# Performance work log

Measured on AMD Instinct MI355X. Metric: run time of the kernel, lower is better.

## Reference

```python
import jax, jax.numpy as jnp
import numpy as np

TOPK = 2


def setup_inputs() -> dict:
    key = jax.random.key(0)
    k1, k2 = jax.random.split(key)
    B, N, D, E, C = 4, 2048, 2048, 8, 512
    token_inputs = jax.random.normal(k1, (B, N, D), dtype=jnp.float32)
    # bottleneck_in.weight.t() stacked over experts: [E, D, C]; scaled like a real init
    bottleneck_weights = jax.random.normal(k2, (E, D, C), dtype=jnp.float32) * 0.02
    return {
        "token_inputs": token_inputs,
        "bottleneck_weights": bottleneck_weights,
        "expert_capacity": 640,
    }


def _routing(router_probs, expert_capacity, topk):
    # router_probs: [B, N, E]
    B, N, E = router_probs.shape
    _, expert_indices = jax.lax.top_k(router_probs, topk)      # [B, N, topk]
    idx = jnp.transpose(expert_indices, (0, 2, 1)).reshape(B, topk * N)
    expert_mask = jax.nn.one_hot(idx, E, dtype=jnp.int32)       # [B, topk*N, E]
    token_priority = jnp.cumsum(expert_mask, axis=1) * expert_mask - 1
    token_priority = token_priority.reshape(B, topk, N, E)
    token_priority = jnp.transpose(token_priority, (0, 2, 1, 3))  # [B, N, topk, E]
    token_priority = jnp.max(token_priority, axis=2)              # [B, N, E]
    # one-hot over capacity; negative (-1) and >= capacity priorities map to all-zero rows
    cap_range = jnp.arange(expert_capacity, dtype=jnp.int32)
    dispatch = (token_priority[..., None] == cap_range).astype(jnp.float32)  # [B,N,E,C]
    combine = router_probs[..., None] * dispatch                            # [B,N,E,C]
    return dispatch, combine


def reference(token_inputs, bottleneck_weights, expert_capacity):
    # activation_cache: [B, N, E, Cb]
    activation_cache = jnp.einsum("bnd,edc->bnec", token_inputs, bottleneck_weights)
    router_logits = jnp.sqrt(jnp.sum(activation_cache * activation_cache, axis=-1))  # [B,N,E]
    router_probs = jax.nn.softmax(router_logits, axis=-1)
    dispatch, combine = _routing(router_probs, expert_capacity, TOPK)
    return jnp.stack([dispatch, combine], axis=0)  # [2, B, N, E, capacity]
```

## Files before the change

kernel.cpp:

```cpp
#include <hip/hip_runtime.h>
#include <math.h>

constexpr int Bb = 4, Nn = 2048, Dd = 2048, Ee = 8, Cbn = 512;
constexpr int Mm = Bb * Nn;
constexpr int Ncols = Ee * Cbn;

typedef _Float16 half8 __attribute__((ext_vector_type(8)));
typedef _Float16 half4v __attribute__((ext_vector_type(4)));
typedef float floatx16 __attribute__((ext_vector_type(16)));

#define GLL16(g, l)                                                     \
  __builtin_amdgcn_global_load_lds(                                     \
      (const __attribute__((address_space(1))) void*)(g),               \
      (__attribute__((address_space(3))) void*)(l), 16, 0, 0)

__global__ __launch_bounds__(256) void split_x(const float* __restrict__ X,
                                               _Float16* __restrict__ hi,
                                               _Float16* __restrict__ lo) {
  int i = (blockIdx.x * 256 + threadIdx.x) * 4;
  float4 v = *(const float4*)(X + i);
  half4v h, l;
  h.x = (_Float16)v.x; l.x = (_Float16)(v.x - (float)h.x);
  h.y = (_Float16)v.y; l.y = (_Float16)(v.y - (float)h.y);
  h.z = (_Float16)v.z; l.z = (_Float16)(v.z - (float)h.z);
  h.w = (_Float16)v.w; l.w = (_Float16)(v.w - (float)h.w);
  *(half4v*)(hi + i) = h;
  *(half4v*)(lo + i) = l;
}

__global__ __launch_bounds__(256) void transpose_w(const float* __restrict__ W,
                                                   _Float16* __restrict__ WThi,
                                                   _Float16* __restrict__ WTlo) {
  const int kt = blockIdx.x;
  const int ct = blockIdx.y;
  const int e = blockIdx.z;
  __shared__ _Float16 thi[64][68];
  __shared__ _Float16 tlo[64][68];
  const int tx = threadIdx.x & 15, ty = threadIdx.x >> 4;
  const float* src = W + ((size_t)(e * 2048 + kt * 64)) * 512 + ct * 64;
#pragma unroll
  for (int p = 0; p < 4; ++p) {
    int kk = ty + p * 16;
    float4 v = *(const float4*)(src + (size_t)kk * 512 + tx * 4);
    _Float16 h;
    h = (_Float16)v.x; thi[tx * 4 + 0][kk] = h; tlo[tx * 4 + 0][kk] = (_Float16)(v.x - (float)h);
    h = (_Float16)v.y; thi[tx * 4 + 1][kk] = h; tlo[tx * 4 + 1][kk] = (_Float16)(v.y - (float)h);
    h = (_Float16)v.z; thi[tx * 4 + 2][kk] = h; tlo[tx * 4 + 2][kk] = (_Float16)(v.z - (float)h);
    h = (_Float16)v.w; thi[tx * 4 + 3][kk] = h; tlo[tx * 4 + 3][kk] = (_Float16)(v.w - (float)h);
  }
  __syncthreads();
  _Float16* dh = WThi + ((size_t)(e * 512 + ct * 64)) * 2048 + kt * 64;
  _Float16* dl = WTlo + ((size_t)(e * 512 + ct * 64)) * 2048 + kt * 64;
#pragma unroll
  for (int p = 0; p < 4; ++p) {
    int cc = ty + p * 16;
    half4v h, l;
    h.x = thi[cc][tx * 4 + 0]; l.x = tlo[cc][tx * 4 + 0];
    h.y = thi[cc][tx * 4 + 1]; l.y = tlo[cc][tx * 4 + 1];
    h.z = thi[cc][tx * 4 + 2]; l.z = tlo[cc][tx * 4 + 2];
    h.w = thi[cc][tx * 4 + 3]; l.w = tlo[cc][tx * 4 + 3];
    *(half4v*)(dh + (size_t)cc * 2048 + tx * 4) = h;
    *(half4v*)(dl + (size_t)cc * 2048 + tx * 4) = l;
  }
}

__global__ __launch_bounds__(256) void gemm_mfma(const _Float16* __restrict__ Xhi,
                                                 const _Float16* __restrict__ Xlo,
                                                 const _Float16* __restrict__ WThi,
                                                 const _Float16* __restrict__ WTlo,
                                                 float* __restrict__ partial) {
  const int mtile = blockIdx.x;
  const int ntile = blockIdx.y;
  const int tid = threadIdx.x;
  const int wave = tid >> 6, lane = tid & 63;
  const int wm = wave >> 1, wn = wave & 1;
  const int h = lane >> 5;

  __shared__ __align__(16) char lds[32768];
  char* ldsAhi = lds;
  char* ldsAlo = lds + 8192;
  char* ldsBhi = lds + 16384;
  char* ldsBlo = lds + 24576;

  const int lr = lane >> 2;
  const int cpos = lane & 3;
  const int cg = cpos ^ ((lr >> 1) & 3);
  const int r0 = wave * 32 + lr;
  const int r1 = r0 + 16;
  const _Float16* xh0 = Xhi + (size_t)(mtile * 128 + r0) * 2048 + cg * 8;
  const _Float16* xh1 = Xhi + (size_t)(mtile * 128 + r1) * 2048 + cg * 8;
  const _Float16* xl0 = Xlo + (size_t)(mtile * 128 + r0) * 2048 + cg * 8;
  const _Float16* xl1 = Xlo + (size_t)(mtile * 128 + r1) * 2048 + cg * 8;
  const _Float16* wh0 = WThi + (size_t)(ntile * 128 + r0) * 2048 + cg * 8;
  const _Float16* wh1 = WThi + (size_t)(ntile * 128 + r1) * 2048 + cg * 8;
  const _Float16* wl0 = WTlo + (size_t)(ntile * 128 + r0) * 2048 + cg * 8;
  const _Float16* wl1 = WTlo + (size_t)(ntile * 128 + r1) * 2048 + cg * 8;
  const int lq0 = wave * 2048;
  const int lq1 = lq0 + 1024;

  const int rA0 = wm * 64 + (lane & 31);
  const int rA1 = rA0 + 32;
  const int rB0 = wn * 64 + (lane & 31);
  const int rB1 = rB0 + 32;
  auto foff = [&](int r, int s) {
    return r * 64 + (((s * 2 + h) ^ ((r >> 1) & 3)) << 4);
  };
  const int oA0[2] = {foff(rA0, 0), foff(rA0, 1)};
  const int oA1[2] = {foff(rA1, 0), foff(rA1, 1)};
  const int oB0[2] = {foff(rB0, 0), foff(rB0, 1)};
  const int oB1[2] = {foff(rB1, 0), foff(rB1, 1)};

  floatx16 acc00 = {}, acc01 = {}, acc10 = {}, acc11 = {};

  for (int kt = 0; kt < 64; ++kt) {
    const int k0 = kt * 32;
    GLL16(xh0 + k0, ldsAhi + lq0);
    GLL16(xh1 + k0, ldsAhi + lq1);
    GLL16(xl0 + k0, ldsAlo + lq0);
    GLL16(xl1 + k0, ldsAlo + lq1);
    GLL16(wh0 + k0, ldsBhi + lq0);
    GLL16(wh1 + k0, ldsBhi + lq1);
    GLL16(wl0 + k0, ldsBlo + lq0);
    GLL16(wl1 + k0, ldsBlo + lq1);
    __syncthreads();
#pragma unroll
    for (int s = 0; s < 2; ++s) {
      half8 ah0 = *(const half8*)(ldsAhi + oA0[s]);
      half8 ah1 = *(const half8*)(ldsAhi + oA1[s]);
      half8 al0 = *(const half8*)(ldsAlo + oA0[s]);
      half8 al1 = *(const half8*)(ldsAlo + oA1[s]);
      half8 bh0 = *(const half8*)(ldsBhi + oB0[s]);
      half8 bh1 = *(const half8*)(ldsBhi + oB1[s]);
      half8 bl0 = *(const half8*)(ldsBlo + oB0[s]);
      half8 bl1 = *(const half8*)(ldsBlo + oB1[s]);
      acc00 = __builtin_amdgcn_mfma_f32_32x32x16_f16(ah0, bh0, acc00, 0, 0, 0);
      acc00 = __builtin_amdgcn_mfma_f32_32x32x16_f16(ah0, bl0, acc00, 0, 0, 0);
      acc00 = __builtin_amdgcn_mfma_f32_32x32x16_f16(al0, bh0, acc00, 0, 0, 0);
      acc01 = __builtin_amdgcn_mfma_f32_32x32x16_f16(ah0, bh1, acc01, 0, 0, 0);
      acc01 = __builtin_amdgcn_mfma_f32_32x32x16_f16(ah0, bl1, acc01, 0, 0, 0);
      acc01 = __builtin_amdgcn_mfma_f32_32x32x16_f16(al0, bh1, acc01, 0, 0, 0);
      acc10 = __builtin_amdgcn_mfma_f32_32x32x16_f16(ah1, bh0, acc10, 0, 0, 0);
      acc10 = __builtin_amdgcn_mfma_f32_32x32x16_f16(ah1, bl0, acc10, 0, 0, 0);
      acc10 = __builtin_amdgcn_mfma_f32_32x32x16_f16(al1, bh0, acc10, 0, 0, 0);
      acc11 = __builtin_amdgcn_mfma_f32_32x32x16_f16(ah1, bh1, acc11, 0, 0, 0);
      acc11 = __builtin_amdgcn_mfma_f32_32x32x16_f16(ah1, bl1, acc11, 0, 0, 0);
      acc11 = __builtin_amdgcn_mfma_f32_32x32x16_f16(al1, bh1, acc11, 0, 0, 0);
    }
    __syncthreads();
  }

  float myv = 0.f;
#pragma unroll
  for (int i = 0; i < 2; ++i) {
    const floatx16& c0 = i ? acc10 : acc00;
    const floatx16& c1 = i ? acc11 : acc01;
#pragma unroll
    for (int reg = 0; reg < 16; ++reg) {
      float v = c0[reg] * c0[reg] + c1[reg] * c1[reg];
#pragma unroll
      for (int m = 1; m <= 16; m <<= 1) v += __shfl_xor(v, m, 64);
      if ((lane & 31) == i * 16 + reg) myv = v;
    }
  }
  {
    const int i = (lane & 31) >> 4;
    const int reg = lane & 15;
    const int row = i * 32 + (reg & 3) + 8 * (reg >> 2) + 4 * h;
    const int token = mtile * 128 + wm * 64 + row;
    const int slice = ntile * 2 + wn;
    partial[(size_t)slice * Mm + token] = myv;
  }
}

__global__ void route_kernel(const float* __restrict__ partial,
                             int* __restrict__ idx1, int* __restrict__ idx2,
                             float* __restrict__ p1, float* __restrict__ p2) {
  int t = blockIdx.x * blockDim.x + threadIdx.x;
  if (t >= Mm) return;
  float l[Ee];
  float mx = -1e30f;
#pragma unroll
  for (int e = 0; e < Ee; ++e) {
    float s = 0.f;
#pragma unroll
    for (int u = 0; u < 8; ++u) s += partial[(size_t)(e * 8 + u) * Mm + t];
    l[e] = sqrtf(s);
    mx = fmaxf(mx, l[e]);
  }
  float p[Ee];
  float s = 0.f;
#pragma unroll
  for (int e = 0; e < Ee; ++e) {
    p[e] = expf(l[e] - mx);
    s += p[e];
  }
  float inv = 1.f / s;
  int i1 = 0;
  float b1 = l[0];
#pragma unroll
  for (int e = 1; e < Ee; ++e)
    if (l[e] > b1) { b1 = l[e]; i1 = e; }
  int i2 = -1;
  float b2 = -1e30f;
#pragma unroll
  for (int e = 0; e < Ee; ++e)
    if (e != i1 && l[e] > b2) { b2 = l[e]; i2 = e; }
  idx1[t] = i1;
  idx2[t] = i2;
  p1[t] = p[i1] * inv;
  p2[t] = p[i2] * inv;
}

__global__ void scan_kernel(const int* __restrict__ idx1,
                            const int* __restrict__ idx2,
                            int* __restrict__ prios) {
  const int b = blockIdx.x;
  const int tid = threadIdx.x;
  __shared__ int cnts[256][8];
  int cnt[8] = {0, 0, 0, 0, 0, 0, 0, 0};
  int eloc[16];
  const int base_p = tid * 16;
#pragma unroll
  for (int i = 0; i < 16; ++i) {
    int p = base_p + i;
    int k = p >> 11;
    int n = p & (Nn - 1);
    int e = (k == 0 ? idx1 : idx2)[b * Nn + n];
    eloc[i] = e;
    cnt[e]++;
  }
#pragma unroll
  for (int e = 0; e < 8; ++e) cnts[tid][e] = cnt[e];
  __syncthreads();
  if (tid < 8) {
    int run = 0;
    for (int i = 0; i < 256; ++i) {
      int v = cnts[i][tid];
      cnts[i][tid] = run;
      run += v;
    }
  }
  __syncthreads();
  int base[8];
#pragma unroll
  for (int e = 0; e < 8; ++e) base[e] = cnts[tid][e];
#pragma unroll
  for (int i = 0; i < 16; ++i) {
    int e = eloc[i];
    prios[b * 2 * Nn + base_p + i] = base[e]++;
  }
}

__global__ void zero_kernel(float4* __restrict__ out, int n4) {
  int i = blockIdx.x * blockDim.x + threadIdx.x;
  if (i < n4) out[i] = make_float4(0.f, 0.f, 0.f, 0.f);
}

__global__ void scatter_kernel(const int* __restrict__ idx1,
                               const int* __restrict__ idx2,
                               const float* __restrict__ p1,
                               const float* __restrict__ p2,
                               const int* __restrict__ prios,
                               float* __restrict__ out, int cap) {
  int t = blockIdx.x * blockDim.x + threadIdx.x;
  if (t >= Mm) return;
  int b = t >> 11;
  int n = t & (Nn - 1);
  size_t disp = (size_t)t * Ee * cap;
  size_t comb = disp + (size_t)Mm * Ee * cap;
  {
    int e = idx1[t];
    int p = prios[b * 2 * Nn + n];
    if (p < cap) {
      out[disp + (size_t)e * cap + p] = 1.f;
      out[comb + (size_t)e * cap + p] = p1[t];
    }
  }
  {
    int e = idx2[t];
    int p = prios[b * 2 * Nn + Nn + n];
    if (p < cap) {
      out[disp + (size_t)e * cap + p] = 1.f;
      out[comb + (size_t)e * cap + p] = p2[t];
    }
  }
}

extern "C" void kernel_launch(void* const* d_in, const int* in_sizes, int n_in,
                              void* d_out, int out_size, void* d_ws, size_t ws_size,
                              hipStream_t stream) {
  const float* X = (const float*)d_in[0];
  const float* W = (const float*)d_in[1];
  float* out = (float*)d_out;
  const int cap = out_size / (2 * Bb * Nn * Ee);

  char* ws = (char*)d_ws;
  _Float16* Xhi = (_Float16*)ws;
  _Float16* Xlo = (_Float16*)(ws + 33554432ull);
  _Float16* WThi = (_Float16*)(ws + 67108864ull);
  _Float16* WTlo = (_Float16*)(ws + 83886080ull);
  float* partial = (float*)(ws + 100663296ull);
  int* idx1 = (int*)(ws + 102760448ull);
  int* idx2 = idx1 + Mm;
  float* p1 = (float*)(idx2 + Mm);
  float* p2 = p1 + Mm;
  int* prios = (int*)(p2 + Mm);

  split_x<<<(Mm * Dd) / 1024, 256, 0, stream>>>(X, Xhi, Xlo);
  transpose_w<<<dim3(32, 8, 8), 256, 0, stream>>>(W, WThi, WTlo);
  gemm_mfma<<<dim3(64, 32), 256, 0, stream>>>(Xhi, Xlo, WThi, WTlo, partial);
  route_kernel<<<Mm / 256, 256, 0, stream>>>(partial, idx1, idx2, p1, p2);
  scan_kernel<<<Bb, 256, 0, stream>>>(idx1, idx2, prios);
  const int n4 = out_size / 4;
  zero_kernel<<<(n4 + 255) / 256, 256, 0, stream>>>((float4*)out, n4);
  scatter_kernel<<<Mm / 256, 256, 0, stream>>>(idx1, idx2, p1, p2, prios, out, cap);
}
```

Before: 820.1 us.

## Double-buffer GEMM LDS, fuse routing into scan, fuse zero-fill with scatter

```diff
diff --git a/kernel.cpp b/kernel.cpp
--- a/kernel.cpp
+++ b/kernel.cpp
@@ -3,7 +3,6 @@
 
 constexpr int Bb = 4, Nn = 2048, Dd = 2048, Ee = 8, Cbn = 512;
 constexpr int Mm = Bb * Nn;
-constexpr int Ncols = Ee * Cbn;
 
 typedef _Float16 half8 __attribute__((ext_vector_type(8)));
 typedef _Float16 half4v __attribute__((ext_vector_type(4)));
@@ -76,11 +75,7 @@
   const int wm = wave >> 1, wn = wave & 1;
   const int h = lane >> 5;
 
-  __shared__ __align__(16) char lds[32768];
-  char* ldsAhi = lds;
-  char* ldsAlo = lds + 8192;
-  char* ldsBhi = lds + 16384;
-  char* ldsBlo = lds + 24576;
+  __shared__ __align__(16) char lds[2][32768];
 
   const int lr = lane >> 2;
   const int cpos = lane & 3;
@@ -112,27 +107,38 @@
 
   floatx16 acc00 = {}, acc01 = {}, acc10 = {}, acc11 = {};
 
+  auto issue = [&](int kt, int buf) {
+    const int k0 = kt * 32;
+    char* L = lds[buf];
+    GLL16(xh0 + k0, L + lq0);
+    GLL16(xh1 + k0, L + lq1);
+    GLL16(xl0 + k0, L + 8192 + lq0);
+    GLL16(xl1 + k0, L + 8192 + lq1);
+    GLL16(wh0 + k0, L + 16384 + lq0);
+    GLL16(wh1 + k0, L + 16384 + lq1);
+    GLL16(wl0 + k0, L + 24576 + lq0);
+    GLL16(wl1 + k0, L + 24576 + lq1);
+  };
+
+  issue(0, 0);
+  int p = 0;
   for (int kt = 0; kt < 64; ++kt) {
-    const int k0 = kt * 32;
-    GLL16(xh0 + k0, ldsAhi + lq0);
-    GLL16(xh1 + k0, ldsAhi + lq1);
-    GLL16(xl0 + k0, ldsAlo + lq0);
-    GLL16(xl1 + k0, ldsAlo + lq1);
-    GLL16(wh0 + k0, ldsBhi + lq0);
-    GLL16(wh1 + k0, ldsBhi + lq1);
-    GLL16(wl0 + k0, ldsBlo + lq0);
-    GLL16(wl1 + k0, ldsBlo + lq1);
     __syncthreads();
+    if (kt < 63) issue(kt + 1, p ^ 1);
+    const char* Ahi = lds[p];
+    const char* Alo = Ahi + 8192;
+    const char* Bhi = Ahi + 16384;
+    const char* Blo = Ahi + 24576;
 #pragma unroll
     for (int s = 0; s < 2; ++s) {
-      half8 ah0 = *(const half8*)(ldsAhi + oA0[s]);
-      half8 ah1 = *(const half8*)(ldsAhi + oA1[s]);
-      half8 al0 = *(const half8*)(ldsAlo + oA0[s]);
-      half8 al1 = *(const half8*)(ldsAlo + oA1[s]);
-      half8 bh0 = *(const half8*)(ldsBhi + oB0[s]);
-      half8 bh1 = *(const half8*)(ldsBhi + oB1[s]);
-      half8 bl0 = *(const half8*)(ldsBlo + oB0[s]);
-      half8 bl1 = *(const half8*)(ldsBlo + oB1[s]);
+      half8 ah0 = *(const half8*)(Ahi + oA0[s]);
+      half8 ah1 = *(const half8*)(Ahi + oA1[s]);
+      half8 al0 = *(const half8*)(Alo + oA0[s]);
+      half8 al1 = *(const half8*)(Alo + oA1[s]);
+      half8 bh0 = *(const half8*)(Bhi + oB0[s]);
+      half8 bh1 = *(const half8*)(Bhi + oB1[s]);
+      half8 bl0 = *(const half8*)(Blo + oB0[s]);
+      half8 bl1 = *(const half8*)(Blo + oB1[s]);
       acc00 = __builtin_amdgcn_mfma_f32_32x32x16_f16(ah0, bh0, acc00, 0, 0, 0);
       acc00 = __builtin_amdgcn_mfma_f32_32x32x16_f16(ah0, bl0, acc00, 0, 0, 0);
       acc00 = __builtin_amdgcn_mfma_f32_32x32x16_f16(al0, bh0, acc00, 0, 0, 0);
@@ -146,7 +152,7 @@
       acc11 = __builtin_amdgcn_mfma_f32_32x32x16_f16(ah1, bl1, acc11, 0, 0, 0);
       acc11 = __builtin_amdgcn_mfma_f32_32x32x16_f16(al1, bh1, acc11, 0, 0, 0);
     }
-    __syncthreads();
+    p ^= 1;
   }
 
   float myv = 0.f;
@@ -172,60 +178,64 @@
   }
 }
 
-__global__ void route_kernel(const float* __restrict__ partial,
-                             int* __restrict__ idx1, int* __restrict__ idx2,
-                             float* __restrict__ p1, float* __restrict__ p2) {
-  int t = blockIdx.x * blockDim.x + threadIdx.x;
-  if (t >= Mm) return;
-  float l[Ee];
-  float mx = -1e30f;
-#pragma unroll
-  for (int e = 0; e < Ee; ++e) {
-    float s = 0.f;
-#pragma unroll
-    for (int u = 0; u < 8; ++u) s += partial[(size_t)(e * 8 + u) * Mm + t];
-    l[e] = sqrtf(s);
-    mx = fmaxf(mx, l[e]);
-  }
-  float p[Ee];
-  float s = 0.f;
-#pragma unroll
-  for (int e = 0; e < Ee; ++e) {
-    p[e] = expf(l[e] - mx);
-    s += p[e];
-  }
-  float inv = 1.f / s;
-  int i1 = 0;
-  float b1 = l[0];
-#pragma unroll
-  for (int e = 1; e < Ee; ++e)
-    if (l[e] > b1) { b1 = l[e]; i1 = e; }
-  int i2 = -1;
-  float b2 = -1e30f;
-#pragma unroll
-  for (int e = 0; e < Ee; ++e)
-    if (e != i1 && l[e] > b2) { b2 = l[e]; i2 = e; }
-  idx1[t] = i1;
-  idx2[t] = i2;
-  p1[t] = p[i1] * inv;
-  p2[t] = p[i2] * inv;
-}
-
-__global__ void scan_kernel(const int* __restrict__ idx1,
-                            const int* __restrict__ idx2,
-                            int* __restrict__ prios) {
+__global__ __launch_bounds__(256) void scan_route(const float* __restrict__ partial,
+                                                  int* __restrict__ ig,
+                                                  float* __restrict__ p1g,
+                                                  float* __restrict__ p2g,
+                                                  int* __restrict__ prios) {
   const int b = blockIdx.x;
   const int tid = threadIdx.x;
+  __shared__ unsigned char sI1[Nn];
+  __shared__ unsigned char sI2[Nn];
   __shared__ int cnts[256][8];
+
+  for (int i = 0; i < 8; ++i) {
+    const int tl = i * 256 + tid;
+    const int t = b * Nn + tl;
+    float l[Ee];
+    float mx = -1e30f;
+#pragma unroll
+    for (int e = 0; e < Ee; ++e) {
+      float s = 0.f;
+#pragma unroll
+      for (int u = 0; u < 8; ++u) s += partial[(size_t)(e * 8 + u) * Mm + t];
+      l[e] = sqrtf(s);
+      mx = fmaxf(mx, l[e]);
+    }
+    float sum = 0.f, pe[Ee];
+#pragma unroll
+    for (int e = 0; e < Ee; ++e) {
+      pe[e] = expf(l[e] - mx);
+      sum += pe[e];
+    }
+    float inv = 1.f / sum;
+    int i1 = 0;
+    float b1 = l[0];
+#pragma unroll
+    for (int e = 1; e < Ee; ++e)
+      if (l[e] > b1) { b1 = l[e]; i1 = e; }
+    int i2 = -1;
+    float b2 = -1e30f;
+#pragma unroll
+    for (int e = 0; e < Ee; ++e)
+      if (e != i1 && l[e] > b2) { b2 = l[e]; i2 = e; }
+    sI1[tl] = (unsigned char)i1;
+    sI2[tl] = (unsigned char)i2;
+    ig[t] = i1 | (i2 << 8);
+    p1g[t] = pe[i1] * inv;
+    p2g[t] = pe[i2] * inv;
+  }
+  __syncthreads();
+
   int cnt[8] = {0, 0, 0, 0, 0, 0, 0, 0};
   int eloc[16];
   const int base_p = tid * 16;
 #pragma unroll
   for (int i = 0; i < 16; ++i) {
-    int p = base_p + i;
-    int k = p >> 11;
-    int n = p & (Nn - 1);
-    int e = (k == 0 ? idx1 : idx2)[b * Nn + n];
+    int pp = base_p + i;
+    int k = pp >> 11;
+    int n = pp & (Nn - 1);
+    int e = k == 0 ? (int)sI1[n] : (int)sI2[n];
     eloc[i] = e;
     cnt[e]++;
   }
@@ -251,38 +261,38 @@
   }
 }
 
-__global__ void zero_kernel(float4* __restrict__ out, int n4) {
-  int i = blockIdx.x * blockDim.x + threadIdx.x;
-  if (i < n4) out[i] = make_float4(0.f, 0.f, 0.f, 0.f);
-}
-
-__global__ void scatter_kernel(const int* __restrict__ idx1,
-                               const int* __restrict__ idx2,
-                               const float* __restrict__ p1,
-                               const float* __restrict__ p2,
-                               const int* __restrict__ prios,
-                               float* __restrict__ out, int cap) {
-  int t = blockIdx.x * blockDim.x + threadIdx.x;
-  if (t >= Mm) return;
-  int b = t >> 11;
-  int n = t & (Nn - 1);
-  size_t disp = (size_t)t * Ee * cap;
-  size_t comb = disp + (size_t)Mm * Ee * cap;
-  {
-    int e = idx1[t];
-    int p = prios[b * 2 * Nn + n];
-    if (p < cap) {
-      out[disp + (size_t)e * cap + p] = 1.f;
-      out[comb + (size_t)e * cap + p] = p1[t];
-    }
-  }
-  {
-    int e = idx2[t];
-    int p = prios[b * 2 * Nn + Nn + n];
-    if (p < cap) {
-      out[disp + (size_t)e * cap + p] = 1.f;
-      out[comb + (size_t)e * cap + p] = p2[t];
-    }
+__global__ __launch_bounds__(256) void out_kernel(const int* __restrict__ ig,
+                                                  const float* __restrict__ p1g,
+                                                  const float* __restrict__ p2g,
+                                                  const int* __restrict__ prios,
+                                                  float* __restrict__ out, int cap) {
+  const int t = blockIdx.x;
+  const int tid = threadIdx.x;
+  const int b = t >> 11, n = t & (Nn - 1);
+  const int pair = ig[t];
+  const int e1 = pair & 0xff, e2 = (pair >> 8) & 0xff;
+  const int q1 = prios[b * 2 * Nn + n];
+  const int q2 = prios[b * 2 * Nn + Nn + n];
+  const float v1 = p1g[t], v2 = p2g[t];
+  const int g1 = (q1 < cap) ? e1 * cap + q1 : -1;
+  const int g2 = (q2 < cap) ? e2 * cap + q2 : -1;
+  const int row4 = Ee * cap / 4;
+  float4* drow = (float4*)out + (size_t)t * row4;
+  float4* crow = drow + (size_t)Mm * row4;
+  for (int f = tid; f < row4; f += 256) {
+    float4 d = make_float4(0.f, 0.f, 0.f, 0.f);
+    float4 c = make_float4(0.f, 0.f, 0.f, 0.f);
+    const int base = f * 4;
+    if (g1 >= base && g1 < base + 4) {
+      ((float*)&d)[g1 - base] = 1.f;
+      ((float*)&c)[g1 - base] = v1;
+    }
+    if (g2 >= base && g2 < base + 4) {
+      ((float*)&d)[g2 - base] = 1.f;
+      ((float*)&c)[g2 - base] = v2;
+    }
+    drow[f] = d;
+    crow[f] = c;
   }
 }
 
@@ -300,18 +310,14 @@
   _Float16* WThi = (_Float16*)(ws + 67108864ull);
   _Float16* WTlo = (_Float16*)(ws + 83886080ull);
   float* partial = (float*)(ws + 100663296ull);
-  int* idx1 = (int*)(ws + 102760448ull);
-  int* idx2 = idx1 + Mm;
-  float* p1 = (float*)(idx2 + Mm);
-  float* p2 = p1 + Mm;
-  int* prios = (int*)(p2 + Mm);
+  int* ig = (int*)(ws + 102760448ull);
+  float* p1g = (float*)(ig + Mm);
+  float* p2g = p1g + Mm;
+  int* prios = (int*)(p2g + Mm);
 
   split_x<<<(Mm * Dd) / 1024, 256, 0, stream>>>(X, Xhi, Xlo);
   transpose_w<<<dim3(32, 8, 8), 256, 0, stream>>>(W, WThi, WTlo);
   gemm_mfma<<<dim3(64, 32), 256, 0, stream>>>(Xhi, Xlo, WThi, WTlo, partial);
-  route_kernel<<<Mm / 256, 256, 0, stream>>>(partial, idx1, idx2, p1, p2);
-  scan_kernel<<<Bb, 256, 0, stream>>>(idx1, idx2, prios);
-  const int n4 = out_size / 4;
-  zero_kernel<<<(n4 + 255) / 256, 256, 0, stream>>>((float4*)out, n4);
-  scatter_kernel<<<Mm / 256, 256, 0, stream>>>(idx1, idx2, p1, p2, prios, out, cap);
-}
+  scan_route<<<Bb, 256, 0, stream>>>(partial, ig, p1g, p2g, prios);
+  out_kernel<<<Mm, 256, 0, stream>>>(ig, p1g, p2g, prios, out, cap);
+}
```

Result: slower. 1.008 ms (+23.0%).
